# Kernel tuning notes

Hardware: AMD Instinct MI355X
Metric: run time of the kernel (lower is better)

## Reference

```python
import jax, jax.numpy as jnp
import numpy as np

B, DIM, H, W = 2, 512, 48, 48
HEADS = 8
HD = DIM // HEADS
NS = 7
R = NS // 2
SCALE = HD ** -0.5
EPS = 1e-12


def _proj(x, w, b):
    # 1x1 conv == channel linear: x [B,C,H,W], w [O,C], b [O]
    return jnp.einsum('bchw,oc->bohw', x, w) + b[None, :, None, None]


def _to_heads(t):
    # [B,C,H,W] -> [B,heads,H,W,head_dim]
    return t.reshape(B, HEADS, HD, H, W).transpose(0, 1, 3, 4, 2)


def setup_inputs() -> dict:
    key = jax.random.key(0)
    ks = jax.random.split(key, 9)
    std = DIM ** -0.5
    inp = {'x': jax.random.normal(ks[0], (B, DIM, H, W), jnp.float32)}
    names = ['wq', 'bq', 'wk', 'bk', 'wv', 'bv', 'wo', 'bo']
    for i, n in enumerate(names):
        if n.startswith('w'):
            inp[n] = jax.random.normal(ks[i + 1], (DIM, DIM), jnp.float32) * std
        else:
            inp[n] = jnp.zeros((DIM,), jnp.float32)
    return inp


def reference(x, wq, bq, wk, bk, wv, bv, wo, bo):
    q = _proj(x, wq, bq)
    k = _proj(x, wk, bk)
    v = _proj(x, wv, bv)
    qh, kh, vh = _to_heads(q), _to_heads(k), _to_heads(v)

    offs = jnp.arange(-R, R + 1)
    oy, ox = jnp.meshgrid(offs, offs, indexing='ij')
    oy, ox = oy.reshape(-1), ox.reshape(-1)  # [K]
    by, bx = jnp.meshgrid(jnp.arange(H), jnp.arange(W), indexing='ij')
    ny = by[..., None] + oy  # [H,W,K]
    nx = bx[..., None] + ox
    valid = (ny >= 0) & (ny < H) & (nx >= 0) & (nx < W)  # [H,W,K]
    ny = jnp.clip(ny, 0, H - 1)
    nx = jnp.clip(nx, 0, W - 1)

    K = NS * NS
    T = H * W
    # gather neighborhoods: [B,heads,H,W,K,head_dim]
    k_nb = kh[:, :, ny, nx].reshape(B, HEADS, T, K, HD)
    v_nb = vh[:, :, ny, nx].reshape(B, HEADS, T, K, HD)
    q_tok = qh.reshape(B, HEADS, T, HD)

    scores = jnp.einsum('bhtd,bhtkd->bhtk', q_tok, k_nb) * SCALE
    neg = jnp.finfo(scores.dtype).min
    scores = jnp.where(valid.reshape(1, 1, T, K), scores, neg)
    attn = jax.nn.softmax(scores, axis=-1)
    out = jnp.einsum('bhtk,bhtkd->bhtd', attn, v_nb)

    # exclude self-value component (self-attention path)
    sv = vh.reshape(B, HEADS, T, HD)
    sv_unit = sv / jnp.maximum(jnp.linalg.norm(sv, axis=-1, keepdims=True), EPS)
    out = out - (out * sv_unit).sum(-1, keepdims=True) * sv_unit

    # [B,heads,T,HD] -> [B,C,H,W]
    out = out.reshape(B, HEADS, H, W, HD).transpose(0, 1, 4, 2, 3).reshape(B, DIM, H, W)
    return _proj(out, wo, bo)
```

## Files before the change

### kernel.cpp

```cpp
#include <hip/hip_runtime.h>
#include <hip/hip_bf16.h>
#include <math.h>

typedef __hip_bfloat16 bf16;
typedef __attribute__((ext_vector_type(4))) float f32x4;
typedef __attribute__((ext_vector_type(8))) short s16x8;
typedef __attribute__((ext_vector_type(4))) short s16x4;

#define B_     2
#define DIM_   512
#define Hh     48
#define Ww     48
#define T_     2304
#define HEADS_ 8
#define HD_    64
#define NS_    7
#define R_     3
#define KK_    49

#define LDSTR  40

__device__ __forceinline__ short f2bs(float f) {
    bf16 h = __float2bfloat16(f);
    return *(short*)&h;
}

__device__ __forceinline__ float bs2f(short s) {
    bf16 h = *reinterpret_cast<const bf16*>(&s);
    return __bfloat162float(h);
}

__device__ __forceinline__ s16x8 cvt8(const float* __restrict__ p) {
    f32x4 a = *(const f32x4*)p;
    f32x4 b = *(const f32x4*)(p + 4);
    s16x8 r;
    r[0] = f2bs(a[0]); r[1] = f2bs(a[1]); r[2] = f2bs(a[2]); r[3] = f2bs(a[3]);
    r[4] = f2bs(b[0]); r[5] = f2bs(b[1]); r[6] = f2bs(b[2]); r[7] = f2bs(b[3]);
    return r;
}

__global__ __launch_bounds__(256) void prep(
    const float* __restrict__ x,
    const float* __restrict__ wq, const float* __restrict__ wk,
    const float* __restrict__ wv, const float* __restrict__ wo,
    bf16* __restrict__ xt, bf16* __restrict__ wb)
{
    __shared__ short tile[64 * 72];
    const int gid = blockIdx.x;
    const int tid = threadIdx.x;

    if (gid < 512) {
        const int i     = gid * 256 + tid;
        const int which = i >> 15;
        const int off   = (i & 32767) * 8;
        const float* src = (which == 0) ? wq : (which == 1) ? wk
                         : (which == 2) ? wv : wo;
        *(s16x8*)((short*)wb + which * 262144 + off) = cvt8(src + off);
        return;
    }

    const int pid = gid - 512;
    const int b   = pid / 288;
    const int rem = pid - b * 288;
    const int t0  = (rem % 36) * 64;
    const int c0  = (rem / 36) * 64;

    const float* X = x + (size_t)b * DIM_ * T_;

    const int c_l = tid >> 4;
    const int t4  = (tid & 15) * 4;
#pragma unroll
    for (int cp = 0; cp < 4; ++cp) {
        const int c = cp * 16 + c_l;
        f32x4 v = *(const f32x4*)(X + (size_t)(c0 + c) * T_ + t0 + t4);
#pragma unroll
        for (int e = 0; e < 4; ++e) tile[(t4 + e) * 72 + c] = f2bs(v[e]);
    }
    __syncthreads();

    const int t_l = tid >> 2;
    const int c16 = (tid & 3) * 16;
    short* dst = (short*)xt + ((size_t)b * T_ + t0 + t_l) * DIM_ + c0 + c16;
    *(s16x8*)(dst)     = *(const s16x8*)(&tile[t_l * 72 + c16]);
    *(s16x8*)(dst + 8) = *(const s16x8*)(&tile[t_l * 72 + c16 + 8]);
}

__global__ __launch_bounds__(256) void gemm_qkv(
    const bf16* __restrict__ xt, const bf16* __restrict__ wb,
    const float* __restrict__ bq, const float* __restrict__ bk,
    const float* __restrict__ bv,
    bf16* __restrict__ qb2, bf16* __restrict__ kb2, bf16* __restrict__ vb2)
{
    const int tt   = blockIdx.x * 128;
    const int ot   = blockIdx.y * 128;
    const int b    = blockIdx.z;
    const int proj = ot >> 9;
    const int orow = ot & 511;
    const int h0   = orow >> 6;

    const float* bsel = (proj == 0) ? bq : (proj == 1) ? bk : bv;
    const short* Wb   = (const short*)wb + proj * 262144;
    const short* X    = (const short*)xt + (size_t)b * T_ * DIM_;
    short*       sel  = (short*)((proj == 0) ? qb2 : (proj == 1) ? kb2 : vb2);

    __shared__ __align__(16) short Xs[128 * LDSTR];
    __shared__ __align__(16) short Ws[128 * LDSTR];

    const int tid  = threadIdx.x;
    const int lane = tid & 63;
    const int wid  = tid >> 6;
    const int ln   = lane & 15;

    const int row = tid >> 2;
    const int cq  = (tid & 3) * 8;

    f32x4 acc[2][8];
#pragma unroll
    for (int r = 0; r < 2; ++r)
#pragma unroll
        for (int n = 0; n < 8; ++n) acc[r][n] = (f32x4){0.f, 0.f, 0.f, 0.f};

    for (int kk = 0; kk < DIM_; kk += 32) {
#pragma unroll
        for (int rr = 0; rr < 2; ++rr) {
            *(s16x8*)(&Xs[(rr * 64 + row) * LDSTR + cq]) =
                *(const s16x8*)(X + (size_t)(tt + rr * 64 + row) * DIM_ + kk + cq);
            *(s16x8*)(&Ws[(rr * 64 + row) * LDSTR + cq]) =
                *(const s16x8*)(Wb + (size_t)(orow + rr * 64 + row) * DIM_ + kk + cq);
        }
        __syncthreads();

        s16x8 a[2];
#pragma unroll
        for (int r = 0; r < 2; ++r)
            a[r] = *(const s16x8*)(&Xs[(r * 64 + wid * 16 + ln) * LDSTR + 8 * (lane >> 4)]);
#pragma unroll
        for (int n = 0; n < 8; ++n) {
            s16x8 bf = *(const s16x8*)(&Ws[(n * 16 + ln) * LDSTR + 8 * (lane >> 4)]);
#pragma unroll
            for (int r = 0; r < 2; ++r)
                acc[r][n] = __builtin_amdgcn_mfma_f32_16x16x32_bf16(a[r], bf, acc[r][n], 0, 0, 0);
        }
        __syncthreads();
    }

    const size_t tb = (size_t)(b * HEADS_ + h0);
#pragma unroll
    for (int r = 0; r < 2; ++r)
#pragma unroll
        for (int n = 0; n < 8; ++n) {
            const int hn   = n >> 2;
            const int d    = (n & 3) * 16 + ln;
            const float bi = bsel[orow + n * 16 + ln];
#pragma unroll
            for (int e = 0; e < 4; ++e) {
                const int t = tt + r * 64 + wid * 16 + (lane >> 4) * 4 + e;
                sel[((tb + hn) * T_ + t) * HD_ + d] = f2bs(acc[r][n][e] + bi);
            }
        }
}

__global__ __launch_bounds__(256) void gemm_out(
    const bf16* __restrict__ ao, const bf16* __restrict__ wb,
    const float* __restrict__ bo, float* __restrict__ out)
{
    const int tt = blockIdx.x * 64;
    const int ot = blockIdx.y * 64;
    const int b  = blockIdx.z;

    const short* X  = (const short*)ao + (size_t)b * T_ * DIM_;
    const short* Wb = (const short*)wb + 3 * 262144;

    __shared__ __align__(16) short Ws[64 * LDSTR];
    __shared__ __align__(16) short Xs[64 * LDSTR];

    const int tid  = threadIdx.x;
    const int lane = tid & 63;
    const int wid  = tid >> 6;

    const int row = tid >> 2;
    const int cq  = (tid & 3) * 8;

    f32x4 acc[4];
#pragma unroll
    for (int n = 0; n < 4; ++n) acc[n] = (f32x4){0.f, 0.f, 0.f, 0.f};

    for (int kk = 0; kk < DIM_; kk += 32) {
        *(s16x8*)(&Ws[row * LDSTR + cq]) =
            *(const s16x8*)(Wb + (size_t)(ot + row) * DIM_ + kk + cq);
        *(s16x8*)(&Xs[row * LDSTR + cq]) =
            *(const s16x8*)(X + (size_t)(tt + row) * DIM_ + kk + cq);
        __syncthreads();

        s16x8 a = *(const s16x8*)(&Ws[(wid * 16 + (lane & 15)) * LDSTR + 8 * (lane >> 4)]);
#pragma unroll
        for (int n = 0; n < 4; ++n) {
            s16x8 bf = *(const s16x8*)(&Xs[(n * 16 + (lane & 15)) * LDSTR + 8 * (lane >> 4)]);
            acc[n] = __builtin_amdgcn_mfma_f32_16x16x32_bf16(a, bf, acc[n], 0, 0, 0);
        }
        __syncthreads();
    }

    float* obase = out + (size_t)b * DIM_ * T_;
#pragma unroll
    for (int n = 0; n < 4; ++n) {
        const int t = tt + n * 16 + (lane & 15);
#pragma unroll
        for (int e = 0; e < 4; ++e) {
            const int o    = ot + wid * 16 + (lane >> 4) * 4 + e;
            obase[(size_t)o * T_ + t] = acc[n][e] + bo[o];
        }
    }
}

__global__ __launch_bounds__(256, 4) void attn_mfma(
    const bf16* __restrict__ qb2, const bf16* __restrict__ kb2,
    const bf16* __restrict__ vb2, bf16* __restrict__ ao)
{
    __shared__ __align__(16) char smem[34048];
    short* Kl = (short*)smem;
    short* Ql = (short*)(smem + 25344);
    short* VT = (short*)smem;
    short* Pl = (short*)(smem + 27648);
    float* Ol = (float*)(smem + 27648);

    const int l   = blockIdx.x;
    const int idx = (l & 7) * 288 + (l >> 3);
    const int bh  = idx / 144;
    const int rem = idx - bh * 144;
    const int y   = rem / 3;
    const int x0  = (rem % 3) * 16;

    const short* qb  = (const short*)qb2 + (size_t)bh * T_ * HD_;
    const short* kb  = (const short*)kb2 + (size_t)bh * T_ * HD_;
    const short* vbb = (const short*)vb2 + (size_t)bh * T_ * HD_;

    const int tid  = threadIdx.x;
    const int lane = tid & 63;
    const int wv   = tid >> 6;
    const int qq   = lane >> 4;
    const int ln   = lane & 15;

    if (tid < 32) {
        const int t = tid >> 1, c = tid & 1;
        *(s16x8*)&Pl[t * 200 + 176 + c * 8] = (s16x8){0,0,0,0,0,0,0,0};
    }
    {
        const int c8 = (tid & 7) * 8;
        const int wr = tid >> 3;
#pragma unroll
        for (int p = 0; p < 6; ++p) {
            const int w = p * 32 + wr;
            if (w < 168) {
                const int wy = w / 24, u = w - wy * 24;
                if (u < 22) {
                    const int gy = min(max(y + wy - 3, 0), 47);
                    const int gx = min(max(x0 + u - 3, 0), 47);
                    *(s16x8*)&Kl[w * 72 + c8] =
                        *(const s16x8*)(kb + (size_t)(gy * 48 + gx) * 64 + c8);
                }
            }
        }
    }
    if (tid < 128) {
        const int t = tid >> 3, c8 = (tid & 7) * 8;
        *(s16x8*)&Ql[t * 72 + c8] =
            *(const s16x8*)(qb + (size_t)(y * 48 + x0 + t) * 64 + c8);
    }
    s16x4 vreg[10];
    {
        const int rr0 = tid >> 4;
        const int d4  = (tid & 15) * 4;
#pragma unroll
        for (int p = 0; p < 10; ++p) {
            const int rr = p * 16 + rr0;
            if (rr < 154) {
                const int wy = rr / 22, u = rr - wy * 22;
                const int gy = min(max(y + wy - 3, 0), 47);
                const int gx = min(max(x0 + u - 3, 0), 47);
                vreg[p] = *(const s16x4*)(vbb + (size_t)(gy * 48 + gx) * 64 + d4);
            }
        }
    }
    __syncthreads();

    f32x4 acc[11];
#pragma unroll
    for (int mt = 0; mt < 11; ++mt) acc[mt] = (f32x4){0.f, 0.f, 0.f, 0.f};
#pragma unroll
    for (int ks = 0; ks < 2; ++ks) {
        s16x8 bq_ = *(const s16x8*)&Ql[ln * 72 + ks * 32 + qq * 8];
#pragma unroll
        for (int mt = 0; mt < 11; ++mt) {
            s16x8 ak = *(const s16x8*)&Kl[(mt * 16 + ln) * 72 + ks * 32 + qq * 8];
            acc[mt] = __builtin_amdgcn_mfma_f32_16x16x32_bf16(ak, bq_, acc[mt], 0, 0, 0);
        }
    }

    const int dx = ln;
    float mxv = -3.0e38f;
#pragma unroll
    for (int mt = 0; mt < 11; ++mt) {
#pragma unroll
        for (int e = 0; e < 4; ++e) {
            const int w  = mt * 16 + qq * 4 + e;
            const int wy = w / 24, u = w - wy * 24;
            const bool valid = (w < 168) &&
                               ((unsigned)(u - dx) <= 6u) &&
                               ((unsigned)(y + wy - 3) < 48u) &&
                               ((unsigned)(x0 + u - 3) < 48u);
            const float s = valid ? acc[mt][e] * 0.125f : -3.0e38f;
            acc[mt][e] = s;
            mxv = fmaxf(mxv, s);
        }
    }
    mxv = fmaxf(mxv, __shfl_xor(mxv, 16));
    mxv = fmaxf(mxv, __shfl_xor(mxv, 32));
    float sum = 0.f;
#pragma unroll
    for (int mt = 0; mt < 11; ++mt)
#pragma unroll
        for (int e = 0; e < 4; ++e) {
            const float p = __expf(acc[mt][e] - mxv);
            acc[mt][e] = p;
            sum += p;
        }
    sum += __shfl_xor(sum, 16);
    sum += __shfl_xor(sum, 32);
    const float inv = 1.0f / sum;

#pragma unroll
    for (int mt = 0; mt < 11; ++mt) {
        const int owner = (mt >= 9) ? 3 : (mt / 3);
        if (wv == owner) {
#pragma unroll
            for (int e = 0; e < 4; ++e) {
                const int w = mt * 16 + qq * 4 + e;
                Pl[ln * 200 + w] = f2bs(acc[mt][e] * inv);
            }
        }
    }
    __syncthreads();

    {
        const int d = tid >> 2, c = tid & 3;
        *(s16x8*)&VT[d * 200 + 168 + c * 8] = (s16x8){0,0,0,0,0,0,0,0};
    }
#pragma unroll
    for (int pp = 0; pp < 2; ++pp) {
        const int r2 = pp * 256 + tid;
        if (r2 < 448) {
            const int wy = r2 >> 6, d = r2 & 63;
            *(unsigned*)&VT[d * 200 + wy * 24 + 22] = 0u;
        }
    }
    {
        const int rr0 = tid >> 4;
        const int d4  = (tid & 15) * 4;
        const int rot = tid & 3;
#pragma unroll
        for (int p = 0; p < 10; ++p) {
            const int rr = p * 16 + rr0;
            if (rr < 154) {
                const int wy = rr / 22, u = rr - wy * 22;
                const int w  = wy * 24 + u;
#pragma unroll
                for (int e = 0; e < 4; ++e) {
                    const int ee = (e + rot) & 3;
                    VT[(d4 + ee) * 200 + w] = vreg[p][ee];
                }
            }
        }
    }
    __syncthreads();

    f32x4 oacc = (f32x4){0.f, 0.f, 0.f, 0.f};
#pragma unroll
    for (int ks = 0; ks < 6; ++ks) {
        s16x8 ap  = *(const s16x8*)&Pl[ln * 200 + ks * 32 + qq * 8];
        s16x8 bv_ = *(const s16x8*)&VT[(wv * 16 + ln) * 200 + ks * 32 + qq * 8];
        oacc = __builtin_amdgcn_mfma_f32_16x16x32_bf16(ap, bv_, oacc, 0, 0, 0);
    }
    __syncthreads();
#pragma unroll
    for (int e = 0; e < 4; ++e)
        Ol[(qq * 4 + e) * 72 + wv * 16 + ln] = oacc[e];
    __syncthreads();

    {
        const int tt = tid >> 4;
        const int dl = tid & 15;
        const int tg = y * 48 + x0 + tt;
        const float o0 = Ol[tt * 72 + dl],      o1 = Ol[tt * 72 + dl + 16],
                    o2 = Ol[tt * 72 + dl + 32], o3 = Ol[tt * 72 + dl + 48];
        const short* vs = vbb + (size_t)tg * 64 + dl;
        const float v0 = bs2f(vs[0]),  v1 = bs2f(vs[16]),
                    v2 = bs2f(vs[32]), v3 = bs2f(vs[48]);
        float n2  = v0 * v0 + v1 * v1 + v2 * v2 + v3 * v3;
        float odv = o0 * v0 + o1 * v1 + o2 * v2 + o3 * v3;
#pragma unroll
        for (int off = 1; off < 16; off <<= 1) {
            n2  += __shfl_xor(n2, off);
            odv += __shfl_xor(odv, off);
        }
        const float mxn = fmaxf(sqrtf(n2), 1e-12f);
        const float cf  = odv / (mxn * mxn);
        const int b = bh >> 3, h = bh & 7;
        bf16* dst = ao + ((size_t)b * T_ + tg) * DIM_ + h * 64 + dl;
        dst[0]  = __float2bfloat16(o0 - cf * v0);
        dst[16] = __float2bfloat16(o1 - cf * v1);
        dst[32] = __float2bfloat16(o2 - cf * v2);
        dst[48] = __float2bfloat16(o3 - cf * v3);
    }
}

extern "C" void kernel_launch(void* const* d_in, const int* in_sizes, int n_in,
                              void* d_out, int out_size, void* d_ws, size_t ws_size,
                              hipStream_t stream)
{
    (void)in_sizes; (void)n_in; (void)out_size; (void)ws_size;

    const float* x  = (const float*)d_in[0];
    const float* wq = (const float*)d_in[1];
    const float* bq = (const float*)d_in[2];
    const float* wk = (const float*)d_in[3];
    const float* bk = (const float*)d_in[4];
    const float* wv = (const float*)d_in[5];
    const float* bv = (const float*)d_in[6];
    const float* wo = (const float*)d_in[7];
    const float* bo = (const float*)d_in[8];
    float* out = (float*)d_out;

    const size_t per = (size_t)B_ * HEADS_ * T_ * HD_;
    bf16* qb2 = (bf16*)d_ws;
    bf16* kb2 = qb2 + per;
    bf16* vb2 = kb2 + per;
    bf16* xa  = vb2 + per;
    bf16* wb  = xa + per;

    prep<<<dim3(512 + 576), 256, 0, stream>>>(x, wq, wk, wv, wo, xa, wb);

    dim3 g1(T_ / 128, 1536 / 128, B_);
    gemm_qkv<<<g1, 256, 0, stream>>>(xa, wb, bq, bk, bv, qb2, kb2, vb2);

    attn_mfma<<<dim3(B_ * HEADS_ * (T_ / 16)), 256, 0, stream>>>(qb2, kb2, vb2, xa);

    dim3 g2(T_ / 64, DIM_ / 64, B_);
    gemm_out<<<g2, 256, 0, stream>>>(xa, wb, bo, out);
}
```

Measured before the change: 66.03 us.

## Enlarge output GEMM tile to 128 rows and drop a barrier in attention

The output projection GEMM now computes 128 output channels per block instead of 64, with each wave holding a 2x4 accumulator grid. This reuses each X tile across twice as many MFMAs and halves the grid size. In the attention kernel the float staging buffer for O moves to its own LDS region so it no longer aliases the P buffer, which lets one __syncthreads be removed. The cost is more LDS per block, which may lower occupancy, and fewer blocks for the GEMM.

New measurement: 72.00 us. +9.0%, slower.

```diff
diff --git a/kernel.cpp b/kernel.cpp
--- a/kernel.cpp
+++ b/kernel.cpp
@@ -165,64 +165,80 @@
     const float* __restrict__ bo, float* __restrict__ out)
 {
     const int tt = blockIdx.x * 64;
-    const int ot = blockIdx.y * 64;
+    const int ot = blockIdx.y * 128;
     const int b  = blockIdx.z;
 
     const short* X  = (const short*)ao + (size_t)b * T_ * DIM_;
     const short* Wb = (const short*)wb + 3 * 262144;
 
-    __shared__ __align__(16) short Ws[64 * LDSTR];
+    __shared__ __align__(16) short Ws[128 * LDSTR];
     __shared__ __align__(16) short Xs[64 * LDSTR];
 
     const int tid  = threadIdx.x;
     const int lane = tid & 63;
-    const int wid  = tid >> 6;
-
-    const int row = tid >> 2;
-    const int cq  = (tid & 3) * 8;
-
-    f32x4 acc[4];
-#pragma unroll
-    for (int n = 0; n < 4; ++n) acc[n] = (f32x4){0.f, 0.f, 0.f, 0.f};
+    const int wv   = tid >> 6;
+    const int ln   = lane & 15;
+    const int qq   = lane >> 4;
+
+    f32x4 acc[2][4];
+#pragma unroll
+    for (int m = 0; m < 2; ++m)
+#pragma unroll
+        for (int n = 0; n < 4; ++n) acc[m][n] = (f32x4){0.f, 0.f, 0.f, 0.f};
 
     for (int kk = 0; kk < DIM_; kk += 32) {
-        *(s16x8*)(&Ws[row * LDSTR + cq]) =
-            *(const s16x8*)(Wb + (size_t)(ot + row) * DIM_ + kk + cq);
-        *(s16x8*)(&Xs[row * LDSTR + cq]) =
-            *(const s16x8*)(X + (size_t)(tt + row) * DIM_ + kk + cq);
+#pragma unroll
+        for (int it = 0; it < 3; ++it) {
+            const int cc  = it * 256 + tid;
+            const int row = cc >> 2;
+            const int c8  = (cc & 3) * 8;
+            if (row < 128)
+                *(s16x8*)(&Ws[row * LDSTR + c8]) =
+                    *(const s16x8*)(Wb + (size_t)(ot + row) * DIM_ + kk + c8);
+            else
+                *(s16x8*)(&Xs[(row - 128) * LDSTR + c8]) =
+                    *(const s16x8*)(X + (size_t)(tt + row - 128) * DIM_ + kk + c8);
+        }
         __syncthreads();
 
-        s16x8 a = *(const s16x8*)(&Ws[(wid * 16 + (lane & 15)) * LDSTR + 8 * (lane >> 4)]);
+        s16x8 a[2];
+#pragma unroll
+        for (int m = 0; m < 2; ++m)
+            a[m] = *(const s16x8*)(&Ws[(wv * 32 + m * 16 + ln) * LDSTR + qq * 8]);
 #pragma unroll
         for (int n = 0; n < 4; ++n) {
-            s16x8 bf = *(const s16x8*)(&Xs[(n * 16 + (lane & 15)) * LDSTR + 8 * (lane >> 4)]);
-            acc[n] = __builtin_amdgcn_mfma_f32_16x16x32_bf16(a, bf, acc[n], 0, 0, 0);
+            s16x8 bf = *(const s16x8*)(&Xs[(n * 16 + ln) * LDSTR + qq * 8]);
+#pragma unroll
+            for (int m = 0; m < 2; ++m)
+                acc[m][n] = __builtin_amdgcn_mfma_f32_16x16x32_bf16(a[m], bf, acc[m][n], 0, 0, 0);
         }
         __syncthreads();
     }
 
     float* obase = out + (size_t)b * DIM_ * T_;
 #pragma unroll
-    for (int n = 0; n < 4; ++n) {
-        const int t = tt + n * 16 + (lane & 15);
-#pragma unroll
-        for (int e = 0; e < 4; ++e) {
-            const int o    = ot + wid * 16 + (lane >> 4) * 4 + e;
-            obase[(size_t)o * T_ + t] = acc[n][e] + bo[o];
-        }
-    }
+    for (int m = 0; m < 2; ++m)
+#pragma unroll
+        for (int n = 0; n < 4; ++n) {
+            const int t = tt + n * 16 + ln;
+#pragma unroll
+            for (int e = 0; e < 4; ++e) {
+                const int o = ot + wv * 32 + m * 16 + qq * 4 + e;
+                obase[(size_t)o * T_ + t] = acc[m][n][e] + bo[o];
+            }
+        }
 }
 
 __global__ __launch_bounds__(256, 4) void attn_mfma(
     const bf16* __restrict__ qb2, const bf16* __restrict__ kb2,
     const bf16* __restrict__ vb2, bf16* __restrict__ ao)
 {
-    __shared__ __align__(16) char smem[34048];
+    __shared__ __align__(16) char smem[38656];
     short* Kl = (short*)smem;
     short* Ql = (short*)(smem + 25344);
     short* VT = (short*)smem;
     short* Pl = (short*)(smem + 27648);
-    float* Ol = (float*)(smem + 27648);
+    float* Ol = (float*)(smem + 34048);
 
     const int l   = blockIdx.x;
     const int idx = (l & 7) * 288 + (l >> 3);
@@ -381,7 +397,6 @@
         s16x8 bv_ = *(const s16x8*)&VT[(wv * 16 + ln) * 200 + ks * 32 + qq * 8];
         oacc = __builtin_amdgcn_mfma_f32_16x16x32_bf16(ap, bv_, oacc, 0, 0, 0);
     }
-    __syncthreads();
 #pragma unroll
     for (int e = 0; e < 4; ++e)
         Ol[(qq * 4 + e) * 72 + wv * 16 + ln] = oacc[e];
@@ -445,6 +460,6 @@
 
     attn_mfma<<<dim3(B_ * HEADS_ * (T_ / 16)), 256, 0, stream>>>(qb2, kb2, vb2, xa);
 
-    dim3 g2(T_ / 64, DIM_ / 64, B_);
+    dim3 g2(T_ / 64, DIM_ / 128, B_);
     gemm_out<<<g2, 256, 0, stream>>>(xa, wb, bo, out);
 }
```
